# Performance work log

Hardware: AMD Instinct MI355X
Metric: run time of the kernel (lower is better)

## Reference

```python
import jax, jax.numpy as jnp
import numpy as np

EPS = 1e-6
HH = 4  # nheads


def _ln(x, g, b):
    mu = jnp.mean(x, axis=-1, keepdims=True)
    var = jnp.mean((x - mu) ** 2, axis=-1, keepdims=True)
    return (x - mu) * jax.lax.rsqrt(var + 1e-5) * g + b


def setup_inputs() -> dict:
    key = jax.random.key(0)
    ks = jax.random.split(key, 12)
    B, T, C, H, W = 4, 32, 128, 32, 32
    Gd = 64
    s_in = 1.0 / np.sqrt(C + Gd)
    s_c = 1.0 / np.sqrt(C)
    s_f = 1.0 / np.sqrt(4 * C)
    return {
        "x": jax.random.normal(ks[0], (B, T, C, H, W), jnp.float32),
        "guidance": jax.random.normal(ks[1], (B, T, Gd), jnp.float32),
        "Wq": jax.random.uniform(ks[2], (C + Gd, C), jnp.float32, -s_in, s_in),
        "bq": jnp.zeros((C,), jnp.float32),
        "Wk": jax.random.uniform(ks[3], (C + Gd, C), jnp.float32, -s_in, s_in),
        "bk": jnp.zeros((C,), jnp.float32),
        "Wv": jax.random.uniform(ks[4], (C, C), jnp.float32, -s_c, s_c),
        "bv": jnp.zeros((C,), jnp.float32),
        "ln1_g": jnp.ones((C,), jnp.float32),
        "ln1_b": jnp.zeros((C,), jnp.float32),
        "ln2_g": jnp.ones((C,), jnp.float32),
        "ln2_b": jnp.zeros((C,), jnp.float32),
        "W1": jax.random.uniform(ks[5], (C, 4 * C), jnp.float32, -s_c, s_c),
        "b1": jnp.zeros((4 * C,), jnp.float32),
        "W2": jax.random.uniform(ks[6], (4 * C, C), jnp.float32, -s_f, s_f),
        "b2": jnp.zeros((C,), jnp.float32),
    }


def reference(x, guidance, Wq, bq, Wk, bk, Wv, bv, ln1_g, ln1_b, ln2_g, ln2_b, W1, b1, W2, b2):
    B, T, C, H, W = x.shape
    Gd = guidance.shape[-1]
    N = B * H * W
    Hd = C // HH
    # (B,T,C,H,W) -> (N,T,C)
    x_bhw = jnp.transpose(x, (0, 3, 4, 1, 2)).reshape(N, T, C)
    g = jnp.broadcast_to(guidance[:, None, None, :, :], (B, H, W, T, Gd)).reshape(N, T, Gd)
    xqk = jnp.concatenate([x_bhw, g], axis=-1)
    q = (xqk @ Wq + bq).reshape(N, T, HH, Hd)
    k = (xqk @ Wk + bk).reshape(N, T, HH, Hd)
    v = (x_bhw @ Wv + bv).reshape(N, T, HH, Hd)
    # elu feature-map linear attention (eval mode, dropout off)
    Q = jax.nn.elu(q) + 1.0
    K = jax.nn.elu(k) + 1.0
    Vn = v / T
    KV = jnp.einsum('nshd,nshv->nhdv', K, Vn)
    Z = 1.0 / (jnp.einsum('nlhd,nhd->nlh', Q, K.sum(axis=1)) + EPS)
    out = jnp.einsum('nlhd,nhdv->nlhv', Q, KV) * Z[..., None] * T
    out = out.reshape(N, T, C)
    out = out + _ln(x_bhw, ln1_g, ln1_b)
    h = _ln(out, ln2_g, ln2_b)
    h = jax.nn.gelu(h @ W1 + b1, approximate=False) @ W2 + b2
    out = out + h
    return jnp.transpose(out.reshape(B, H, W, T, C), (0, 3, 4, 1, 2))
```

## Files before the change

kernel.cpp:

```cpp
#include <hip/hip_runtime.h>
#include <hip/hip_bf16.h>
#include <math.h>

#define T_   32
#define C_   128
#define GD_  64
#define KQK_ 192
#define NH_  4
#define HD_  32
#define C4_  512
#define HW_  1024

typedef unsigned short u16;
typedef __attribute__((ext_vector_type(8))) short short8;
typedef __attribute__((ext_vector_type(4))) short short4v;
typedef __attribute__((ext_vector_type(4))) float f32x4;
typedef __attribute__((ext_vector_type(4))) unsigned short u16x4;

#define ACF_A 0
#define ACF_C 512
#define WQH 2048
#define WQL 26624
#define WKH 51200
#define WKL 75776
#define WVH 100352
#define WVL 116736
#define W1H 133120
#define W1L 198656
#define W2H 264192
#define W2L 329728
#define GSH 395264
#define GSL 403456
#define XT  411648
#define WS_NEED_BYTES (823296ull + 4096ull*8192ull*2ull)

#define AX_H  0
#define AX_L  25600
#define X2G(g) ((g)*8704)
#define HM_H  34816
#define HM_L  52224
#define KSUM  69632
#define ZDEN  70656
#define STATS 71680
#define LN2P  72704
#define POOLB 74752

__device__ __forceinline__ float b2f(u16 u) {
    unsigned int x = ((unsigned int)u) << 16;
    float f; __builtin_memcpy(&f, &x, 4); return f;
}
__device__ __forceinline__ u16 f2b(float f) {
    __hip_bfloat16 h = __float2bfloat16(f);
    u16 u; __builtin_memcpy(&u, &h, 2); return u;
}
__device__ __forceinline__ void split2(float v, u16& h, u16& l) {
    h = f2b(v); l = f2b(v - b2f(h));
}
__device__ __forceinline__ void splitfrag(const f32x4 v, short4v& h, short4v& l) {
    u16 hh[4], ll[4];
    #pragma unroll
    for (int r = 0; r < 4; ++r) { hh[r] = f2b(v[r]); ll[r] = f2b(v[r] - b2f(hh[r])); }
    h = (short4v){(short)hh[0],(short)hh[1],(short)hh[2],(short)hh[3]};
    l = (short4v){(short)ll[0],(short)ll[1],(short)ll[2],(short)ll[3]};
}

__device__ __forceinline__ float gelu_fast(float v) {
    float a  = fabsf(v) * 0.70710678118654752f;
    float t  = __builtin_amdgcn_rcpf(fmaf(a, 0.3275911f, 1.f));
    float p  = t*(0.254829592f + t*(-0.284496736f + t*(1.421413741f
             + t*(-1.453152027f + t*1.061405429f))));
    float P  = p * __expf(-a*a);
    float hv = 0.5f * v;
    return (v > 0.f) ? v - hv*P : hv*P;
}

__device__ __forceinline__ f32x4 mfma16(short4v a, short4v b, f32x4 c) {
#if __has_builtin(__builtin_amdgcn_mfma_f32_16x16x16bf16_1k)
    return __builtin_amdgcn_mfma_f32_16x16x16bf16_1k(a, b, c, 0, 0, 0);
#else
    asm("v_mfma_f32_16x16x16_bf16 %0, %1, %2, %0" : "+v"(c) : "v"(a), "v"(b));
    return c;
#endif
}

#define MFMA3(acc, ah, al, bh, bl)                                          \
    acc = __builtin_amdgcn_mfma_f32_16x16x32_bf16(ah, bh, acc, 0, 0, 0);    \
    acc = __builtin_amdgcn_mfma_f32_16x16x32_bf16(ah, bl, acc, 0, 0, 0);    \
    acc = __builtin_amdgcn_mfma_f32_16x16x32_bf16(al, bh, acc, 0, 0, 0);

#define MFMA3_16(acc, ah, al, bh, bl)                                       \
    acc = mfma16(ah, bh, acc);                                              \
    acc = mfma16(ah, bl, acc);                                              \
    acc = mfma16(al, bh, acc);

__global__ void prep_weights(const float* __restrict__ Wq, const float* __restrict__ Wk,
                             const float* __restrict__ Wv, const float* __restrict__ W1,
                             const float* __restrict__ W2, const float* __restrict__ gui,
                             const float* __restrict__ g2, const float* __restrict__ be2,
                             const float* __restrict__ b1,
                             u16* __restrict__ wsp)
{
    int e = blockIdx.x * 256 + threadIdx.x;
    if (e >= 204800) {
        int n = e - 204800;
        if (n >= 512) return;
        float a = 0.f, c = 0.f;
        for (int k = 0; k < 128; ++k) {
            float w = W1[k*512 + n];
            a = fmaf(w, g2[k], a);
            c = fmaf(w, be2[k], c);
        }
        float* acf = (float*)wsp;
        acf[ACF_A + n] = a;
        acf[ACF_C + n] = c + b1[n];
        return;
    }
    if (e >= 196608) {
        int idx = e - 196608;
        float v = gui[idx];
        u16 hb = f2b(v);
        wsp[GSH + idx] = hb;
        wsp[GSL + idx] = f2b(v - b2f(hb));
        return;
    }
    const float* src; int e2, k, n, K; int oh, ol; int isW1 = 0;
    if (e < 24576)       { src = Wq; e2 = e;          k = e2 >> 7; n = e2 & 127; K = KQK_; oh = WQH; ol = WQL; }
    else if (e < 49152)  { src = Wk; e2 = e - 24576;  k = e2 >> 7; n = e2 & 127; K = KQK_; oh = WKH; ol = WKL; }
    else if (e < 65536)  { src = Wv; e2 = e - 49152;  k = e2 >> 7; n = e2 & 127; K = C_;   oh = WVH; ol = WVL; }
    else if (e < 131072) { src = W1; e2 = e - 65536;  k = e2 >> 9; n = e2 & 511; K = C_;   oh = W1H; ol = W1L; isW1 = 1; }
    else                 { src = W2; e2 = e - 131072; k = e2 >> 7; n = e2 & 127; K = C4_;  oh = W2H; ol = W2L; }
    float w = src[e2];
    if (isW1) w *= g2[k];
    u16 hb = f2b(w);
    wsp[oh + n * K + k] = hb;
    wsp[ol + n * K + k] = f2b(w - b2f(hb));
}

__global__ __launch_bounds__(256) void transpose_x(const float* __restrict__ x, u16* __restrict__ wsp)
{
    __shared__ float tile[32][65];
    int bid = blockIdx.x;
    int hq = bid & 15, cq = (bid >> 4) & 3, t = (bid >> 6) & 31, b = bid >> 11;
    int c0 = cq * 32, hw0 = hq * 64;
    int tid = threadIdx.x;
    {
        int i = tid >> 3, j8 = (tid & 7) * 8;
        const float* src = x + ((size_t)((b*32 + t)*128 + c0 + i))*1024 + hw0 + j8;
        float4 v0 = *reinterpret_cast<const float4*>(src);
        float4 v1 = *reinterpret_cast<const float4*>(src + 4);
        tile[i][j8+0]=v0.x; tile[i][j8+1]=v0.y; tile[i][j8+2]=v0.z; tile[i][j8+3]=v0.w;
        tile[i][j8+4]=v1.x; tile[i][j8+5]=v1.y; tile[i][j8+6]=v1.z; tile[i][j8+7]=v1.w;
    }
    __syncthreads();
    {
        int jj = tid >> 2, c8 = (tid & 3) * 8;
        int n = b*1024 + hw0 + jj;
        u16 hh[8], ll[8];
        #pragma unroll
        for (int ii = 0; ii < 8; ++ii) {
            float v = tile[c8 + ii][jj];
            u16 hb = f2b(v);
            hh[ii] = hb; ll[ii] = f2b(v - b2f(hb));
        }
        u16* dh = wsp + XT + (size_t)n*8192 + t*128 + c0 + c8;
        u16* dl = dh + 4096;
        *reinterpret_cast<ushort4*>(dh)     = make_ushort4(hh[0],hh[1],hh[2],hh[3]);
        *reinterpret_cast<ushort4*>(dh + 4) = make_ushort4(hh[4],hh[5],hh[6],hh[7]);
        *reinterpret_cast<ushort4*>(dl)     = make_ushort4(ll[0],ll[1],ll[2],ll[3]);
        *reinterpret_cast<ushort4*>(dl + 4) = make_ushort4(ll[4],ll[5],ll[6],ll[7]);
    }
}

__global__ __launch_bounds__(256, 2) void fused_linattn_mfma(
    const float* __restrict__ x,
    const float* __restrict__ bq, const float* __restrict__ bk, const float* __restrict__ bv,
    const float* __restrict__ g1, const float* __restrict__ be1,
    const float* __restrict__ b2,
    const u16* __restrict__ wsp, int use_xt,
    float* __restrict__ out)
{
    extern __shared__ __align__(16) char pool[];
    float* ksum  = (float*)(pool + KSUM);
    float* zf    = (float*)(pool + ZDEN);
    float* stats = (float*)(pool + STATS);
    float* ln2p  = (float*)(pool + LN2P);
    const float* acf = (const float*)wsp;

    const int bi  = blockIdx.x;
    const int j_  = ((bi & 7) << 8) | (bi >> 3);
    const int n0  = j_ * 2;
    const int b   = n0 >> 10;
    const int hw0 = n0 & 1023;
    const int tid = threadIdx.x;
    const int lane = tid & 63, wv = tid >> 6;
    const int l16  = lane & 15, quad = lane >> 4;

    short8 wqh[6][2], wql[6][2];
    #pragma unroll
    for (int ks = 0; ks < 6; ++ks)
        #pragma unroll
        for (int nt = 0; nt < 2; ++nt) {
            const int n = (wv*2 + nt)*16 + l16;
            wqh[ks][nt] = *(const short8*)(wsp + WQH + n*KQK_ + ks*32 + quad*8);
            wql[ks][nt] = *(const short8*)(wsp + WQL + n*KQK_ + ks*32 + quad*8);
        }

    if (use_xt) {
        #pragma unroll
        for (int tau = 0; tau < 2; ++tau) {
            const u16* xtb = wsp + XT + (size_t)(n0 + tau) * 8192;
            #pragma unroll
            for (int i = 0; i < 2; ++i) {
                int off = (tid + i*256) * 8;
                int t = off >> 7, c = off & 127;
                short8 vh = *reinterpret_cast<const short8*>(xtb + off);
                short8 vl = *reinterpret_cast<const short8*>(xtb + 4096 + off);
                *reinterpret_cast<short8*>(pool + AX_H + (tau*32 + t)*400 + c*2) = vh;
                *reinterpret_cast<short8*>(pool + AX_L + (tau*32 + t)*400 + c*2) = vl;
            }
        }
    } else {
        #pragma unroll
        for (int tau = 0; tau < 2; ++tau) {
            const float* xb = x + (size_t)b * (T_*C_*HW_) + hw0 + tau;
            #pragma unroll
            for (int i = 0; i < 16; ++i) {
                int idx = tid + i*256;
                float v = xb[(size_t)idx * HW_];
                int t = idx >> 7, c = idx & 127;
                u16 hb = f2b(v);
                *(u16*)(pool + AX_H + (tau*32 + t)*400 + c*2) = hb;
                *(u16*)(pool + AX_L + (tau*32 + t)*400 + c*2) = f2b(v - b2f(hb));
            }
        }
    }
    {
        const u16* gh = wsp + GSH + b*2048 + tid*8;
        const u16* gl = wsp + GSL + b*2048 + tid*8;
        int off = tid * 8;
        int t = off >> 6, jg = off & 63;
        short8 vh = *reinterpret_cast<const short8*>(gh);
        short8 vl = *reinterpret_cast<const short8*>(gl);
        *reinterpret_cast<short8*>(pool + AX_H + t*400 + 256 + jg*2) = vh;
        *reinterpret_cast<short8*>(pool + AX_L + t*400 + 256 + jg*2) = vl;
        *reinterpret_cast<short8*>(pool + AX_H + (32 + t)*400 + 256 + jg*2) = vh;
        *reinterpret_cast<short8*>(pool + AX_L + (32 + t)*400 + 256 + jg*2) = vl;
    }
    __syncthreads();

    short4v qfh[4][2], qfl[4][2];
    short4v kfh[4][2], kfl[4][2];
    short4v vfh[4][2], vfl[4][2];

    {
        f32x4 aq[4][2];
        #pragma unroll
        for (int mt = 0; mt < 4; ++mt)
            #pragma unroll
            for (int nt = 0; nt < 2; ++nt) aq[mt][nt] = (f32x4){0.f,0.f,0.f,0.f};
        #pragma unroll
        for (int ks = 0; ks < 6; ++ks) {
            short8 ah[4], al[4];
            #pragma unroll
            for (int mt = 0; mt < 4; ++mt) {
                ah[mt] = *(const short8*)(pool + AX_H + (mt*16 + l16)*400 + ks*64 + quad*16);
                al[mt] = *(const short8*)(pool + AX_L + (mt*16 + l16)*400 + ks*64 + quad*16);
            }
            #pragma unroll
            for (int nt = 0; nt < 2; ++nt)
                #pragma unroll
                for (int mt = 0; mt < 4; ++mt) { MFMA3(aq[mt][nt], wqh[ks][nt], wql[ks][nt], ah[mt], al[mt]); }
        }
        #pragma unroll
        for (int ct = 0; ct < 2; ++ct) {
            f32x4 bq4 = *(const f32x4*)(bq + wv*32 + ct*16 + quad*4);
            #pragma unroll
            for (int mt = 0; mt < 4; ++mt) {
                f32x4 qp;
                #pragma unroll
                for (int r = 0; r < 4; ++r) {
                    float q = aq[mt][ct][r] + bq4[r];
                    qp[r] = (q > 0.f) ? q + 1.f : __expf(q);
                }
                splitfrag(qp, qfh[mt][ct], qfl[mt][ct]);
            }
        }
    }

    {
        f32x4 ak[4][2];
        #pragma unroll
        for (int mt = 0; mt < 4; ++mt)
            #pragma unroll
            for (int nt = 0; nt < 2; ++nt) ak[mt][nt] = (f32x4){0.f,0.f,0.f,0.f};
        #pragma unroll
        for (int ks = 0; ks < 6; ++ks) {
            short8 ah[4], al[4];
            #pragma unroll
            for (int mt = 0; mt < 4; ++mt) {
                ah[mt] = *(const short8*)(pool + AX_H + (mt*16 + l16)*400 + ks*64 + quad*16);
                al[mt] = *(const short8*)(pool + AX_L + (mt*16 + l16)*400 + ks*64 + quad*16);
            }
            #pragma unroll
            for (int nt = 0; nt < 2; ++nt) {
                const int n = (wv*2 + nt)*16 + l16;
                short8 bh = *(const short8*)(wsp + WKH + n*KQK_ + ks*32 + quad*8);
                short8 bl = *(const short8*)(wsp + WKL + n*KQK_ + ks*32 + quad*8);
                #pragma unroll
                for (int mt = 0; mt < 4; ++mt) { MFMA3(ak[mt][nt], ah[mt], al[mt], bh, bl); }
            }
        }
        float sk[2][2] = {{0.f,0.f},{0.f,0.f}};
        #pragma unroll
        for (int nt = 0; nt < 2; ++nt) {
            float bias = bk[wv*32 + nt*16 + l16];
            #pragma unroll
            for (int mt = 0; mt < 4; ++mt) {
                f32x4 kp;
                #pragma unroll
                for (int r = 0; r < 4; ++r) {
                    float k = ak[mt][nt][r] + bias;
                    float v = (k > 0.f) ? k + 1.f : __expf(k);
                    kp[r] = v;
                    sk[mt >> 1][nt] += v;
                }
                splitfrag(kp, kfh[mt][nt], kfl[mt][nt]);
            }
        }
        #pragma unroll
        for (int tau = 0; tau < 2; ++tau)
            #pragma unroll
            for (int nt = 0; nt < 2; ++nt) {
                float s = sk[tau][nt];
                s += __shfl_xor(s, 16); s += __shfl_xor(s, 32);
                if (quad == 0) ksum[tau*128 + wv*32 + nt*16 + l16] = s;
            }
    }

    {
        f32x4 av[4][2];
        #pragma unroll
        for (int mt = 0; mt < 4; ++mt)
            #pragma unroll
            for (int nt = 0; nt < 2; ++nt) av[mt][nt] = (f32x4){0.f,0.f,0.f,0.f};
        #pragma unroll
        for (int ks = 0; ks < 4; ++ks) {
            short8 ah[4], al[4];
            #pragma unroll
            for (int mt = 0; mt < 4; ++mt) {
                ah[mt] = *(const short8*)(pool + AX_H + (mt*16 + l16)*400 + ks*64 + quad*16);
                al[mt] = *(const short8*)(pool + AX_L + (mt*16 + l16)*400 + ks*64 + quad*16);
            }
            #pragma unroll
            for (int nt = 0; nt < 2; ++nt) {
                const int n = (wv*2 + nt)*16 + l16;
                short8 bh = *(const short8*)(wsp + WVH + n*C_ + ks*32 + quad*8);
                short8 bl = *(const short8*)(wsp + WVL + n*C_ + ks*32 + quad*8);
                #pragma unroll
                for (int mt = 0; mt < 4; ++mt) { MFMA3(av[mt][nt], ah[mt], al[mt], bh, bl); }
            }
        }
        #pragma unroll
        for (int nt = 0; nt < 2; ++nt) {
            float bias = bv[wv*32 + nt*16 + l16];
            #pragma unroll
            for (int mt = 0; mt < 4; ++mt) {
                f32x4 vp;
                #pragma unroll
                for (int r = 0; r < 4; ++r) vp[r] = av[mt][nt][r] + bias;
                splitfrag(vp, vfh[mt][nt], vfl[mt][nt]);
            }
        }
    }

    #pragma unroll
    for (int tau = 0; tau < 2; ++tau) {
        f32x4 ka0 = *(const f32x4*)(ksum + tau*128 + wv*32 + quad*4);
        f32x4 ka1 = *(const f32x4*)(ksum + tau*128 + wv*32 + 16 + quad*4);
        #pragma unroll
        for (int lt = 0; lt < 2; ++lt) {
            const int mt = tau*2 + lt;
            float p = 0.f;
            #pragma unroll
            for (int i = 0; i < 4; ++i) {
                p = fmaf(b2f((u16)(short)qfh[mt][0][i]) + b2f((u16)(short)qfl[mt][0][i]), ka0[i], p);
                p = fmaf(b2f((u16)(short)qfh[mt][1][i]) + b2f((u16)(short)qfl[mt][1][i]), ka1[i], p);
            }
            p += __shfl_xor(p, 16); p += __shfl_xor(p, 32);
            if (quad == 0) zf[tau*128 + wv*32 + lt*16 + l16] = 1.f / (p + 1e-6f);
        }
    }

    short4v kvfh[2][2][2], kvfl[2][2][2];
    #pragma unroll
    for (int tau = 0; tau < 2; ++tau)
        #pragma unroll
        for (int dt = 0; dt < 2; ++dt)
            #pragma unroll
            for (int vt = 0; vt < 2; ++vt) {
                f32x4 kv = (f32x4){0.f,0.f,0.f,0.f};
                #pragma unroll
                for (int lt = 0; lt < 2; ++lt) {
                    const int mt = tau*2 + lt;
                    MFMA3_16(kv, kfh[mt][dt], kfl[mt][dt], vfh[mt][vt], vfl[mt][vt]);
                }
                splitfrag(kv, kvfh[tau][dt][vt], kvfl[tau][dt][vt]);
            }

    {
        int t = tid >> 2, jj = tid & 3;
        const char* rp = pool + AX_H + t*400 + jj*64;
        float m = 0.f, s = 0.f;
        #pragma unroll
        for (int p8 = 0; p8 < 4; ++p8) {
            short8 h = *(const short8*)(rp + p8*16);
            short8 l = *(const short8*)(rp + (AX_L - AX_H) + p8*16);
            #pragma unroll
            for (int i = 0; i < 8; ++i) {
                float v = b2f((u16)h[i]) + b2f((u16)l[i]);
                m += v; s = fmaf(v, v, s);
            }
        }
        m += __shfl_xor(m, 1); s += __shfl_xor(s, 1);
        m += __shfl_xor(m, 2); s += __shfl_xor(s, 2);
        if (jj == 0) {
            float mu = m * (1.f/C_);
            stats[t]      = mu;
            stats[64 + t] = rsqrtf(s * (1.f/C_) - mu*mu + 1e-5f);
        }
    }
    __syncthreads();

    f32x4 o1v[4][2];
    #pragma unroll
    for (int mt = 0; mt < 4; ++mt) {
        const int tau = mt >> 1;
        f32x4 zd4 = *(const f32x4*)(zf + tau*128 + wv*32 + (mt & 1)*16 + quad*4);
        f32x4 mu4 = *(const f32x4*)(stats + mt*16 + quad*4);
        f32x4 rs4 = *(const f32x4*)(stats + 64 + mt*16 + quad*4);
        #pragma unroll
        for (int vt = 0; vt < 2; ++vt) {
            f32x4 oa = (f32x4){0.f,0.f,0.f,0.f};
            #pragma unroll
            for (int dt = 0; dt < 2; ++dt) {
                MFMA3_16(oa, qfh[mt][dt], qfl[mt][dt], kvfh[tau][dt][vt], kvfl[tau][dt][vt]);
            }
            int ch = wv*32 + vt*16 + l16;
            float g1c = g1[ch], be1c = be1[ch];
            #pragma unroll
            for (int r = 0; r < 4; ++r) {
                int row = mt*16 + quad*4 + r;
                float xv = b2f(*(const u16*)(pool + AX_H + row*400 + ch*2))
                         + b2f(*(const u16*)(pool + AX_L + row*400 + ch*2));
                o1v[mt][vt][r] = oa[r]*zd4[r] + (xv - mu4[r])*rs4[r]*g1c + be1c;
            }
        }
    }
    {
        #pragma unroll
        for (int mt = 0; mt < 4; ++mt)
            #pragma unroll
            for (int r = 0; r < 4; ++r) {
                float v0 = o1v[mt][0][r], v1 = o1v[mt][1][r];
                float m = v0 + v1;
                float s = v0*v0 + v1*v1;
                m += __shfl_xor(m, 1); s += __shfl_xor(s, 1);
                m += __shfl_xor(m, 2); s += __shfl_xor(s, 2);
                m += __shfl_xor(m, 4); s += __shfl_xor(s, 4);
                m += __shfl_xor(m, 8); s += __shfl_xor(s, 8);
                if (l16 == 0) {
                    int row = mt*16 + quad*4 + r;
                    ln2p[wv*64 + row]       = m;
                    ln2p[256 + wv*64 + row] = s;
                }
            }
    }
    __syncthreads();

    #pragma unroll
    for (int mt = 0; mt < 4; ++mt) {
        char* xb = pool + X2G(mt);
        #pragma unroll
        for (int vt = 0; vt < 2; ++vt) {
            int ch = wv*32 + vt*16 + l16;
            #pragma unroll
            for (int r = 0; r < 4; ++r) {
                u16 hb, lb; split2(o1v[mt][vt][r], hb, lb);
                int off = (quad*4 + r)*272 + ch*2;
                *(u16*)(xb + off)        = hb;
                *(u16*)(xb + 4352 + off) = lb;
            }
        }
    }
    if (tid < 64) {
        int t = tid;
        float m = 0.f, s = 0.f;
        #pragma unroll
        for (int w = 0; w < 4; ++w) { m += ln2p[w*64 + t]; s += ln2p[256 + w*64 + t]; }
        float mu = m * (1.f/C_);
        float rs = rsqrtf(s * (1.f/C_) - mu*mu + 1e-5f);
        stats[128 + t] = mu * rs;
        stats[192 + t] = rs;
    }
    __syncthreads();

    f32x4 accO[4][2];
    #pragma unroll
    for (int mt = 0; mt < 4; ++mt)
        #pragma unroll
        for (int nt = 0; nt < 2; ++nt) accO[mt][nt] = (f32x4){0.f,0.f,0.f,0.f};

    #pragma unroll 1
    for (int mh = 0; mh < 4; ++mh) {
        {
            f32x4 accH[4][2];
            #pragma unroll
            for (int mt = 0; mt < 4; ++mt)
                #pragma unroll
                for (int nt = 0; nt < 2; ++nt) accH[mt][nt] = (f32x4){0.f,0.f,0.f,0.f};
            #pragma unroll
            for (int ks = 0; ks < 4; ++ks) {
                short8 ah[4], al[4];
                #pragma unroll
                for (int mt = 0; mt < 4; ++mt) {
                    const char* xb = pool + X2G(mt) + l16*272 + ks*64 + quad*16;
                    ah[mt] = *(const short8*)(xb);
                    al[mt] = *(const short8*)(xb + 4352);
                }
                #pragma unroll
                for (int nt = 0; nt < 2; ++nt) {
                    const int gn = mh*128 + (wv*2 + nt)*16 + l16;
                    short8 bh = *(const short8*)(wsp + W1H + gn*C_ + ks*32 + quad*8);
                    short8 bl = *(const short8*)(wsp + W1L + gn*C_ + ks*32 + quad*8);
                    #pragma unroll
                    for (int mt = 0; mt < 4; ++mt) { MFMA3(accH[mt][nt], bh, bl, ah[mt], al[mt]); }
                }
            }
            #pragma unroll
            for (int nt = 0; nt < 2; ++nt) {
                int base = mh*128 + (wv*2 + nt)*16 + quad*4;
                f32x4 a4 = *(const f32x4*)(acf + ACF_A + base);
                f32x4 c4 = *(const f32x4*)(acf + ACF_C + base);
                int ch0 = (wv*2 + nt)*16 + quad*4;
                #pragma unroll
                for (int mt = 0; mt < 4; ++mt) {
                    int tk = mt*16 + l16;
                    float mrs = stats[128 + tk], rsv = stats[192 + tk];
                    u16 hh[4], ll[4];
                    #pragma unroll
                    for (int r = 0; r < 4; ++r) {
                        float v = accH[mt][nt][r]*rsv - mrs*a4[r] + c4[r];
                        float ge = gelu_fast(v);
                        split2(ge, hh[r], ll[r]);
                    }
                    char* hb = pool + HM_H + tk*272 + ch0*2;
                    *(u16x4*)(hb)                    = (u16x4){hh[0],hh[1],hh[2],hh[3]};
                    *(u16x4*)(hb + (HM_L - HM_H))    = (u16x4){ll[0],ll[1],ll[2],ll[3]};
                }
            }
        }
        __syncthreads();
        {
            #pragma unroll
            for (int ks = 0; ks < 4; ++ks) {
                short8 ah[4], al[4];
                #pragma unroll
                for (int mt = 0; mt < 4; ++mt) {
                    const char* hb = pool + HM_H + (mt*16 + l16)*272 + ks*64 + quad*16;
                    ah[mt] = *(const short8*)(hb);
                    al[mt] = *(const short8*)(hb + (HM_L - HM_H));
                }
                #pragma unroll
                for (int nt = 0; nt < 2; ++nt) {
                    const int n = (wv*2 + nt)*16 + l16;
                    short8 bh = *(const short8*)(wsp + W2H + n*C4_ + mh*128 + ks*32 + quad*8);
                    short8 bl = *(const short8*)(wsp + W2L + n*C4_ + mh*128 + ks*32 + quad*8);
                    #pragma unroll
                    for (int mt = 0; mt < 4; ++mt) { MFMA3(accO[mt][nt], ah[mt], al[mt], bh, bl); }
                }
            }
        }
        if (mh < 3) __syncthreads();
    }

    {
        float* obase = out + (size_t)b * (T_*C_*HW_) + hw0;
        #pragma unroll
        for (int mt = 0; mt < 4; ++mt) {
            const int tau = mt >> 1;
            float* ob = obase + tau;
            #pragma unroll
            for (int nt = 0; nt < 2; ++nt) {
                int ch = wv*32 + nt*16 + l16;
                float b2c = b2[ch];
                #pragma unroll
                for (int r = 0; r < 4; ++r) {
                    int t = (mt & 1)*16 + quad*4 + r;
                    float y = o1v[mt][nt][r] + accO[mt][nt][r] + b2c;
                    ob[(size_t)(t*C_ + ch) * HW_] = y;
                }
            }
        }
    }
}

extern "C" void kernel_launch(void* const* d_in, const int* in_sizes, int n_in,
                              void* d_out, int out_size, void* d_ws, size_t ws_size,
                              hipStream_t stream)
{
    const float* x   = (const float*)d_in[0];
    const float* gui = (const float*)d_in[1];
    const float* Wq  = (const float*)d_in[2];
    const float* bq  = (const float*)d_in[3];
    const float* Wk  = (const float*)d_in[4];
    const float* bk  = (const float*)d_in[5];
    const float* Wv  = (const float*)d_in[6];
    const float* bv  = (const float*)d_in[7];
    const float* g1  = (const float*)d_in[8];
    const float* be1 = (const float*)d_in[9];
    const float* g2  = (const float*)d_in[10];
    const float* be2 = (const float*)d_in[11];
    const float* W1  = (const float*)d_in[12];
    const float* b1  = (const float*)d_in[13];
    const float* W2  = (const float*)d_in[14];
    const float* b2  = (const float*)d_in[15];
    u16* wsp = (u16*)d_ws;

    int use_xt = (ws_size >= WS_NEED_BYTES) ? 1 : 0;

    prep_weights<<<dim3(802), dim3(256), 0, stream>>>(Wq, Wk, Wv, W1, W2, gui, g2, be2, b1, wsp);
    if (use_xt)
        transpose_x<<<dim3(8192), dim3(256), 0, stream>>>(x, wsp);

    (void)hipFuncSetAttribute((const void*)fused_linattn_mfma,
                              hipFuncAttributeMaxDynamicSharedMemorySize,
                              POOLB);
    fused_linattn_mfma<<<dim3(2048), dim3(256), POOLB, stream>>>(
        x, bq, bk, bv, g1, be1, b2, wsp, use_xt, (float*)d_out);
}
```

Before: 428.9 us.

## Split fused attention+MLP kernel into two kernels for higher occupancy

The single fused kernel becomes an attention kernel and an MLP kernel. The attention kernel writes its hi/lo bf16 split output into the XT workspace region, overwriting x there. The MLP kernel then reloads it, one position per block, recomputes the LN2 stats and runs the FFN. The aim is more blocks in flight through smaller LDS pools and fewer accumulator registers (launch bounds 3 and 4). The cost is an extra global round trip of the intermediate, plus a second launch. The XT write path appears to assume use_xt is enabled, so if the workspace is too small the MLP kernel would read unwritten memory.

```diff
diff --git a/kernel.cpp b/kernel.cpp
--- a/kernel.cpp
+++ b/kernel.cpp
@@ -37,13 +37,15 @@
 #define AX_H  0
 #define AX_L  25600
 #define X2G(g) ((g)*8704)
-#define HM_H  34816
-#define HM_L  52224
-#define KSUM  69632
-#define ZDEN  70656
-#define STATS 71680
-#define LN2P  72704
-#define POOLB 74752
+#define KSUM  51200
+#define ZDEN  52224
+#define STATS 53248
+#define POOLA 53760
+
+#define BX2   0
+#define BHM   17408
+#define BST   34816
+#define POOLB 35072
 
 __device__ __forceinline__ float b2f(u16 u) {
     unsigned int x = ((unsigned int)u) << 16;
@@ -171,20 +173,16 @@
     }
 }
 
-__global__ __launch_bounds__(256, 2) void fused_linattn_mfma(
+__global__ __launch_bounds__(256, 3) void attn_mfma(
     const float* __restrict__ x,
     const float* __restrict__ bq, const float* __restrict__ bk, const float* __restrict__ bv,
     const float* __restrict__ g1, const float* __restrict__ be1,
-    const float* __restrict__ b2,
-    const u16* __restrict__ wsp, int use_xt,
-    float* __restrict__ out)
+    u16* __restrict__ wsp, int use_xt)
 {
     extern __shared__ __align__(16) char pool[];
     float* ksum  = (float*)(pool + KSUM);
     float* zf    = (float*)(pool + ZDEN);
     float* stats = (float*)(pool + STATS);
-    float* ln2p  = (float*)(pool + LN2P);
-    const float* acf = (const float*)wsp;
 
     const int bi  = blockIdx.x;
     const int j_  = ((bi & 7) << 8) | (bi >> 3);
@@ -456,25 +454,6 @@
             }
         }
     }
-    {
-        #pragma unroll
-        for (int mt = 0; mt < 4; ++mt)
-            #pragma unroll
-            for (int r = 0; r < 4; ++r) {
-                float v0 = o1v[mt][0][r], v1 = o1v[mt][1][r];
-                float m = v0 + v1;
-                float s = v0*v0 + v1*v1;
-                m += __shfl_xor(m, 1); s += __shfl_xor(s, 1);
-                m += __shfl_xor(m, 2); s += __shfl_xor(s, 2);
-                m += __shfl_xor(m, 4); s += __shfl_xor(s, 4);
-                m += __shfl_xor(m, 8); s += __shfl_xor(s, 8);
-                if (l16 == 0) {
-                    int row = mt*16 + quad*4 + r;
-                    ln2p[wv*64 + row]       = m;
-                    ln2p[256 + wv*64 + row] = s;
-                }
-            }
-    }
     __syncthreads();
 
     #pragma unroll
@@ -492,40 +471,105 @@
             }
         }
     }
-    if (tid < 64) {
-        int t = tid;
+    __syncthreads();
+
+    {
+        u16* dst = wsp + XT + (size_t)n0 * 8192;
+        #pragma unroll
+        for (int i = 0; i < 8; ++i) {
+            int cid = tid + i*256;
+            int tau = cid >> 10;
+            int rem = cid & 1023;
+            int plane = rem >> 9;
+            int rr = (rem >> 4) & 31;
+            int c8 = (rem & 15) << 3;
+            int grow = tau*32 + rr;
+            const char* lsrc = pool + X2G(grow >> 4) + plane*4352 + (grow & 15)*272 + c8*2;
+            short8 v = *reinterpret_cast<const short8*>(lsrc);
+            *reinterpret_cast<short8*>(dst + (size_t)tau*8192 + plane*4096 + rr*128 + c8) = v;
+        }
+    }
+}
+
+__global__ __launch_bounds__(256, 4) void mlp_mfma(
+    const float* __restrict__ b2, const u16* __restrict__ wsp,
+    float* __restrict__ out)
+{
+    extern __shared__ __align__(16) char pool[];
+    float* stats = (float*)(pool + BST);
+    const float* acf = (const float*)wsp;
+
+    const int bi = blockIdx.x;
+    const int n  = ((bi & 7) << 9) | (bi >> 3);
+    const int b  = n >> 10;
+    const int hw = n & 1023;
+    const int tid = threadIdx.x;
+    const int lane = tid & 63, wv = tid >> 6;
+    const int l16 = lane & 15, quad = lane >> 4;
+
+    {
+        const u16* src = wsp + XT + (size_t)n * 8192;
+        #pragma unroll
+        for (int i = 0; i < 4; ++i) {
+            int cid = tid + i*256;
+            int plane = cid >> 9;
+            int rr = (cid >> 4) & 31;
+            int c8 = (cid & 15) << 3;
+            short8 v = *reinterpret_cast<const short8*>(src + plane*4096 + rr*128 + c8);
+            *reinterpret_cast<short8*>(pool + BX2 + plane*8704 + rr*272 + c8*2) = v;
+        }
+    }
+    __syncthreads();
+
+    {
+        int row = tid >> 3, j = tid & 7;
+        const char* rp = pool + BX2 + row*272 + j*32;
+        short8 h0 = *(const short8*)(rp);
+        short8 h1 = *(const short8*)(rp + 16);
+        short8 l0 = *(const short8*)(rp + 8704);
+        short8 l1 = *(const short8*)(rp + 8704 + 16);
         float m = 0.f, s = 0.f;
         #pragma unroll
-        for (int w = 0; w < 4; ++w) { m += ln2p[w*64 + t]; s += ln2p[256 + w*64 + t]; }
-        float mu = m * (1.f/C_);
-        float rs = rsqrtf(s * (1.f/C_) - mu*mu + 1e-5f);
-        stats[128 + t] = mu * rs;
-        stats[192 + t] = rs;
+        for (int i = 0; i < 8; ++i) {
+            float v = b2f((u16)h0[i]) + b2f((u16)l0[i]);
+            m += v; s = fmaf(v, v, s);
+            v = b2f((u16)h1[i]) + b2f((u16)l1[i]);
+            m += v; s = fmaf(v, v, s);
+        }
+        m += __shfl_xor(m, 1); s += __shfl_xor(s, 1);
+        m += __shfl_xor(m, 2); s += __shfl_xor(s, 2);
+        m += __shfl_xor(m, 4); s += __shfl_xor(s, 4);
+        if (j == 0) {
+            float mu = m * (1.f/C_);
+            float rs = rsqrtf(s * (1.f/C_) - mu*mu + 1e-5f);
+            stats[row]      = mu * rs;
+            stats[32 + row] = rs;
+        }
     }
     __syncthreads();
 
-    f32x4 accO[4][2];
+    f32x4 accO[2][2];
     #pragma unroll
-    for (int mt = 0; mt < 4; ++mt)
+    for (int mt = 0; mt < 2; ++mt)
         #pragma unroll
         for (int nt = 0; nt < 2; ++nt) accO[mt][nt] = (f32x4){0.f,0.f,0.f,0.f};
 
     #pragma unroll 1
     for (int mh = 0; mh < 4; ++mh) {
         {
-            f32x4 accH[4][2];
-            #pragma unroll
-            for (int mt = 0; mt < 4; ++mt)
+            f32x4 accH[2][2];
+            #pragma unroll
+            for (int mt = 0; mt < 2; ++mt)
                 #pragma unroll
                 for (int nt = 0; nt < 2; ++nt) accH[mt][nt] = (f32x4){0.f,0.f,0.f,0.f};
             #pragma unroll
             for (int ks = 0; ks < 4; ++ks) {
-                short8 ah[4], al[4];
-                #pragma unroll
-                for (int mt = 0; mt < 4; ++mt) {
-                    const char* xb = pool + X2G(mt) + l16*272 + ks*64 + quad*16;
+                short8 ah[2], al[2];
+                #pragma unroll
+                for (int mt = 0; mt < 2; ++mt) {
+                    const char* xb = pool + BX2 + (mt*16 + l16)*272 + ks*64 + quad*16;
                     ah[mt] = *(const short8*)(xb);
-                    al[mt] = *(const short8*)(xb + 4352);
+                    al[mt] = *(const short8*)(xb + 8704);
                 }
                 #pragma unroll
                 for (int nt = 0; nt < 2; ++nt) {
@@ -533,7 +577,7 @@
                     short8 bh = *(const short8*)(wsp + W1H + gn*C_ + ks*32 + quad*8);
                     short8 bl = *(const short8*)(wsp + W1L + gn*C_ + ks*32 + quad*8);
                     #pragma unroll
-                    for (int mt = 0; mt < 4; ++mt) { MFMA3(accH[mt][nt], bh, bl, ah[mt], al[mt]); }
+                    for (int mt = 0; mt < 2; ++mt) { MFMA3(accH[mt][nt], bh, bl, ah[mt], al[mt]); }
                 }
             }
             #pragma unroll
@@ -543,9 +587,9 @@
                 f32x4 c4 = *(const f32x4*)(acf + ACF_C + base);
                 int ch0 = (wv*2 + nt)*16 + quad*4;
                 #pragma unroll
-                for (int mt = 0; mt < 4; ++mt) {
+                for (int mt = 0; mt < 2; ++mt) {
                     int tk = mt*16 + l16;
-                    float mrs = stats[128 + tk], rsv = stats[192 + tk];
+                    float mrs = stats[tk], rsv = stats[32 + tk];
                     u16 hh[4], ll[4];
                     #pragma unroll
                     for (int r = 0; r < 4; ++r) {
@@ -553,9 +597,9 @@
                         float ge = gelu_fast(v);
                         split2(ge, hh[r], ll[r]);
                     }
-                    char* hb = pool + HM_H + tk*272 + ch0*2;
-                    *(u16x4*)(hb)                    = (u16x4){hh[0],hh[1],hh[2],hh[3]};
-                    *(u16x4*)(hb + (HM_L - HM_H))    = (u16x4){ll[0],ll[1],ll[2],ll[3]};
+                    char* hb = pool + BHM + tk*272 + ch0*2;
+                    *(u16x4*)(hb)        = (u16x4){hh[0],hh[1],hh[2],hh[3]};
+                    *(u16x4*)(hb + 8704) = (u16x4){ll[0],ll[1],ll[2],ll[3]};
                 }
             }
         }
@@ -563,20 +607,20 @@
         {
             #pragma unroll
             for (int ks = 0; ks < 4; ++ks) {
-                short8 ah[4], al[4];
-                #pragma unroll
-                for (int mt = 0; mt < 4; ++mt) {
-                    const char* hb = pool + HM_H + (mt*16 + l16)*272 + ks*64 + quad*16;
+                short8 ah[2], al[2];
+                #pragma unroll
+                for (int mt = 0; mt < 2; ++mt) {
+                    const char* hb = pool + BHM + (mt*16 + l16)*272 + ks*64 + quad*16;
                     ah[mt] = *(const short8*)(hb);
-                    al[mt] = *(const short8*)(hb + (HM_L - HM_H));
+                    al[mt] = *(const short8*)(hb + 8704);
                 }
                 #pragma unroll
                 for (int nt = 0; nt < 2; ++nt) {
-                    const int n = (wv*2 + nt)*16 + l16;
-                    short8 bh = *(const short8*)(wsp + W2H + n*C4_ + mh*128 + ks*32 + quad*8);
-                    short8 bl = *(const short8*)(wsp + W2L + n*C4_ + mh*128 + ks*32 + quad*8);
+                    const int n2 = (wv*2 + nt)*16 + l16;
+                    short8 bh = *(const short8*)(wsp + W2H + n2*C4_ + mh*128 + ks*32 + quad*8);
+                    short8 bl = *(const short8*)(wsp + W2L + n2*C4_ + mh*128 + ks*32 + quad*8);
                     #pragma unroll
-                    for (int mt = 0; mt < 4; ++mt) { MFMA3(accO[mt][nt], ah[mt], al[mt], bh, bl); }
+                    for (int mt = 0; mt < 2; ++mt) { MFMA3(accO[mt][nt], ah[mt], al[mt], bh, bl); }
                 }
             }
         }
@@ -584,19 +628,19 @@
     }
 
     {
-        float* obase = out + (size_t)b * (T_*C_*HW_) + hw0;
-        #pragma unroll
-        for (int mt = 0; mt < 4; ++mt) {
-            const int tau = mt >> 1;
-            float* ob = obase + tau;
+        float* ob = out + (size_t)b * (T_*C_*HW_) + hw;
+        #pragma unroll
+        for (int mt = 0; mt < 2; ++mt) {
             #pragma unroll
             for (int nt = 0; nt < 2; ++nt) {
                 int ch = wv*32 + nt*16 + l16;
                 float b2c = b2[ch];
                 #pragma unroll
                 for (int r = 0; r < 4; ++r) {
-                    int t = (mt & 1)*16 + quad*4 + r;
-                    float y = o1v[mt][nt][r] + accO[mt][nt][r] + b2c;
+                    int t = mt*16 + quad*4 + r;
+                    float o1 = b2f(*(const u16*)(pool + BX2 + t*272 + ch*2))
+                             + b2f(*(const u16*)(pool + BX2 + 8704 + t*272 + ch*2));
+                    float y = o1 + accO[mt][nt][r] + b2c;
                     ob[(size_t)(t*C_ + ch) * HW_] = y;
                 }
             }
@@ -632,9 +676,13 @@
     if (use_xt)
         transpose_x<<<dim3(8192), dim3(256), 0, stream>>>(x, wsp);
 
-    (void)hipFuncSetAttribute((const void*)fused_linattn_mfma,
-                              hipFuncAttributeMaxDynamicSharedMemorySize,
-                              POOLB);
-    fused_linattn_mfma<<<dim3(2048), dim3(256), POOLB, stream>>>(
-        x, bq, bk, bv, g1, be1, b2, wsp, use_xt, (float*)d_out);
-}
+    (void)hipFuncSetAttribute((const void*)attn_mfma,
+                              hipFuncAttributeMaxDynamicSharedMemorySize, POOLA);
+    (void)hipFuncSetAttribute((const void*)mlp_mfma,
+                              hipFuncAttributeMaxDynamicSharedMemorySize, POOLB);
+
+    attn_mfma<<<dim3(2048), dim3(256), POOLA, stream>>>(
+        x, bq, bk, bv, g1, be1, wsp, use_xt);
+    mlp_mfma<<<dim3(4096), dim3(256), POOLB, stream>>>(
+        b2, wsp, (float*)d_out);
+}
```

After: 563.2 us. 31.3% more time.
